# Performance work log

Hardware: AMD Instinct MI355X
Metric: run time of the kernel (lower is better)

The kernel has to match this reference:

```python
import jax, jax.numpy as jnp
import numpy as np

H, DH, D, S, B = 8, 64, 512, 512, 2
EPS = 1e-5

def _trop_linear(x, W):
    # y[..., o] = max_i (x[..., i] + W[o, i])
    return jnp.max(x[..., None, :] + W, axis=-1)

def _layer_norm(x, gamma, beta):
    mu = jnp.mean(x, axis=-1, keepdims=True)
    var = jnp.mean((x - mu) ** 2, axis=-1, keepdims=True)
    return (x - mu) * jax.lax.rsqrt(var + EPS) * gamma + beta

def setup_inputs() -> dict:
    key = jax.random.key(0)
    ks = jax.random.split(key, 8)
    sc = lambda fan_in: 1.0 / np.sqrt(fan_in)
    return {
        "h":   jax.random.normal(ks[0], (S, B, D), jnp.float32),
        "Wq":  jax.random.normal(ks[1], (H * DH, D), jnp.float32) * sc(D),
        "Wkv": jax.random.normal(ks[2], (2 * H * DH, D), jnp.float32) * sc(D),
        "Wqt": jax.random.normal(ks[3], (DH, DH), jnp.float32),
        "Wkt": jax.random.normal(ks[4], (DH, DH), jnp.float32),
        "Wvt": jax.random.normal(ks[5], (DH, DH), jnp.float32),
        "lam": jnp.ones((1, 1, D), jnp.float32),
        "Wo":  jax.random.normal(ks[6], (D, H * DH), jnp.float32) * sc(H * DH),
        "gamma": jnp.ones((D,), jnp.float32),
        "beta":  jnp.zeros((D,), jnp.float32),
    }

def reference(h, Wq, Wkv, Wqt, Wkt, Wvt, lam, Wo, gamma, beta):
    # h: [S, B, D]; mems=None so c == h; pre_lnorm=False
    c = h
    head_q = h @ Wq.T                                # [S, B, H*DH]
    kv = c @ Wkv.T                                   # [S, B, 2*H*DH]
    head_k, head_v = jnp.split(kv, 2, axis=-1)

    norm = lambda x: jnp.log1p(jax.nn.relu(x)) - lam  # tropical normalize
    head_q, head_k, head_v = norm(head_q), norm(head_k), norm(head_v)

    # [S,B,H,DH] -> [B,S,H,DH] -> flat reshape to [B*H, S, DH] (matches torch)
    to_bh = lambda x: jnp.transpose(x.reshape(S, B, H, DH), (1, 0, 2, 3)).reshape(B * H, S, DH)
    q = _trop_linear(to_bh(head_q), Wqt)
    k = _trop_linear(to_bh(head_k), Wkt)
    v = _trop_linear(to_bh(head_v), Wvt)

    # tropical distance score: -(max_d(q-k) - min_d(q-k)) over head dim
    diff = q[:, :, None, :] - k[:, None, :, :]        # [BH, Sq, Sk, DH]
    attn_scores = -(jnp.max(diff, axis=-1) - jnp.min(diff, axis=-1))  # [BH,Sq,Sk]

    # max-plus aggregation: context = max_sk(score + v)
    sum_sv = attn_scores[..., None] + v[:, None, :, :]  # [BH, Sq, Sk, DH]
    context = jnp.max(sum_sv, axis=2)                   # [BH, Sq, DH]

    # flat reshape back (matches torch), permute, expm1
    context = context.reshape(B, H, S, DH)
    context = jnp.transpose(context, (2, 0, 1, 3))      # [S, B, H, DH]
    context = jnp.expm1(context)
    attn_vec = context.reshape(S, B, H * DH)

    attn_out = attn_vec @ Wo.T                          # [S, B, D]
    return _layer_norm(h + attn_out, gamma, beta)
```

## Files before the change

### kernel.cpp

```cpp
#include <hip/hip_runtime.h>
#include <cmath>

typedef __attribute__((ext_vector_type(8))) __bf16 bf16x8;
typedef __attribute__((ext_vector_type(4))) float f32x4;

namespace {
constexpr int GP = 512;
constexpr int WS_Q = 0;
constexpr int WS_K = 524288;
constexpr int WS_V = 1048576;
}

__device__ inline unsigned short f2bf(float x) {
  union { float f; unsigned u; } v; v.f = x;
  unsigned r = v.u + 0x7fff + ((v.u >> 16) & 1);
  return (unsigned short)(r >> 16);
}

__device__ inline void cvt8_store(unsigned short* dst, float4 a, float4 b) {
  ushort4 lo, hi;
  lo.x = f2bf(a.x); lo.y = f2bf(a.y); lo.z = f2bf(a.z); lo.w = f2bf(a.w);
  hi.x = f2bf(b.x); hi.y = f2bf(b.y); hi.z = f2bf(b.z); hi.w = f2bf(b.w);
  *(ushort4*)dst = lo; *(ushort4*)(dst + 4) = hi;
}

__global__ __launch_bounds__(256) void k_gemm0t(const float* __restrict__ h,
    const float* __restrict__ Wq, const float* __restrict__ Wkv,
    const float* __restrict__ lam, const float* __restrict__ Wqt,
    const float* __restrict__ Wkt, const float* __restrict__ Wvt,
    float* __restrict__ qkv)
{
  __shared__ unsigned short As[64][72];
  __shared__ unsigned short Bs[64][72];
  __shared__ float Wl[64][65];
  __shared__ float nl[64][68];
  const int tid = threadIdx.x;
  const int bx = blockIdx.x;
  const int r0 = blockIdx.y * 64, c0 = bx * 64;
  const int which = c0 >> 9;
  const int hh = bx & 7;
  const float* Wt = (which == 0) ? Wqt : (which == 1) ? Wkt : Wvt;
  #pragma unroll
  for (int q = 0; q < 16; ++q) {
    int idx = q * 256 + tid;
    Wl[idx >> 6][idx & 63] = Wt[idx];
  }
  const int w = tid >> 6, l = tid & 63;
  const int wr = (w >> 1) * 32, wc = (w & 1) * 32;
  const int srow = tid >> 3, sk8 = (tid & 7) * 8;
  f32x4 acc[2][2] = {};
  for (int kk = 0; kk < 512; kk += 64) {
    __syncthreads();
    #pragma unroll
    for (int q2 = 0; q2 < 2; ++q2) {
      int row = srow + q2 * 32;
      const float* ap = &h[(r0 + row) * 512 + kk + sk8];
      cvt8_store(&As[row][sk8], *(const float4*)ap, *(const float4*)(ap + 4));
      int c = c0 + row;
      const float* wrp = (c < 512) ? (Wq + c * 512) : (Wkv + (c - 512) * 512);
      cvt8_store(&Bs[row][sk8], *(const float4*)&wrp[kk + sk8],
                 *(const float4*)&wrp[kk + sk8 + 4]);
    }
    __syncthreads();
    #pragma unroll
    for (int ks = 0; ks < 2; ++ks) {
      const int kc = ks * 32 + (l >> 4) * 8;
      bf16x8 a0 = *(const bf16x8*)&As[wr +      (l & 15)][kc];
      bf16x8 a1 = *(const bf16x8*)&As[wr + 16 + (l & 15)][kc];
      bf16x8 b0 = *(const bf16x8*)&Bs[wc +      (l & 15)][kc];
      bf16x8 b1 = *(const bf16x8*)&Bs[wc + 16 + (l & 15)][kc];
      acc[0][0] = __builtin_amdgcn_mfma_f32_16x16x32_bf16(a0, b0, acc[0][0], 0, 0, 0);
      acc[0][1] = __builtin_amdgcn_mfma_f32_16x16x32_bf16(a0, b1, acc[0][1], 0, 0, 0);
      acc[1][0] = __builtin_amdgcn_mfma_f32_16x16x32_bf16(a1, b0, acc[1][0], 0, 0, 0);
      acc[1][1] = __builtin_amdgcn_mfma_f32_16x16x32_bf16(a1, b1, acc[1][1], 0, 0, 0);
    }
  }
  #pragma unroll
  for (int i = 0; i < 2; ++i)
    #pragma unroll
    for (int j = 0; j < 2; ++j)
      #pragma unroll
      for (int r = 0; r < 4; ++r) {
        int rl = wr + i * 16 + (l >> 4) * 4 + r;
        int cl = wc + j * 16 + (l & 15);
        nl[rl][cl] = log1pf(fmaxf(acc[i][j][r], 0.f)) - lam[hh * 64 + cl];
      }
  __syncthreads();
  float wreg[64];
  #pragma unroll
  for (int i = 0; i < 64; ++i) wreg[i] = Wl[l][i];
  #pragma unroll 2
  for (int it = 0; it < 16; ++it) {
    int lr = w + it * 4;
    float m0 = -INFINITY, m1 = -INFINITY, m2 = -INFINITY, m3 = -INFINITY;
    #pragma unroll
    for (int i = 0; i < 64; i += 4) {
      f32x4 nv = *(const f32x4*)&nl[lr][i];
      m0 = fmaxf(m0, nv[0] + wreg[i]);
      m1 = fmaxf(m1, nv[1] + wreg[i + 1]);
      m2 = fmaxf(m2, nv[2] + wreg[i + 2]);
      m3 = fmaxf(m3, nv[3] + wreg[i + 3]);
    }
    int r = r0 + lr;
    int s = r >> 1, bb = r & 1;
    int g = bb * 8 + (s >> 6);
    int p = ((s & 63) << 3) | hh;
    qkv[which * 524288 + ((g << 9) + p) * 64 + l] =
        fmaxf(fmaxf(m0, m1), fmaxf(m2, m3));
  }
}

__global__ __launch_bounds__(256) void k_attn(const float* __restrict__ qkv,
    float* __restrict__ ctxp)
{
  const int pt = blockIdx.x;
  const int g  = blockIdx.y;
  const int cs = blockIdx.z;
  const float* qb = qkv + WS_Q + g * GP * 64;
  const float* kb = qkv + WS_K + g * GP * 64;
  const float* vb = qkv + WS_V + g * GP * 64;
  __shared__ float qs[32][64];
  __shared__ float ks[64][64];
  __shared__ float vs[64][64];
  __shared__ float ss[32][68];
  const int tid = threadIdx.x;
  const int tr = tid >> 4, tc = tid & 15;
  const int xb = tc & 7;
  #pragma unroll
  for (int q2 = 0; q2 < 2; ++q2) {
    int row = tr + q2 * 16;
    f32x4 v4 = *(const f32x4*)&qb[(pt * 32 + row) * 64 + tc * 4];
    *(f32x4*)&qs[row][((tc ^ (row & 7))) * 4] = v4;
  }
  float ctx[2][4];
  #pragma unroll
  for (int i = 0; i < 2; ++i)
    #pragma unroll
    for (int j = 0; j < 4; ++j) ctx[i][j] = -INFINITY;

  for (int cc = 0; cc < 2; ++cc) {
    const int c0 = cs * 128 + cc * 64;
    __syncthreads();
    #pragma unroll
    for (int q4 = 0; q4 < 4; ++q4) {
      int row = tr + q4 * 16;
      int sb = (tc ^ (row & 7)) * 4;
      *(f32x4*)&ks[row][sb] = *(const f32x4*)&kb[(c0 + row) * 64 + tc * 4];
      *(f32x4*)&vs[row][sb] = *(const f32x4*)&vb[(c0 + row) * 64 + tc * 4];
    }
    __syncthreads();
    float mx[2][4], mn[2][4];
    #pragma unroll
    for (int i = 0; i < 2; ++i)
      #pragma unroll
      for (int m = 0; m < 4; ++m) { mx[i][m] = -INFINITY; mn[i][m] = INFINITY; }
    const int r0 = tr * 2, r1 = r0 + 1;
    #pragma unroll 2
    for (int b = 0; b < 16; ++b) {
      f32x4 q0 = *(const f32x4*)&qs[r0][(b ^ (r0 & 7)) * 4];
      f32x4 q1 = *(const f32x4*)&qs[r1][(b ^ (r1 & 7)) * 4];
      const int kblk = (b ^ xb) * 4;
      #pragma unroll
      for (int m = 0; m < 4; ++m) {
        f32x4 kv = *(const f32x4*)&ks[tc + m * 16][kblk];
        #pragma unroll
        for (int e = 0; e < 4; ++e) {
          float d0 = q0[e] - kv[e];
          float d1 = q1[e] - kv[e];
          mx[0][m] = fmaxf(mx[0][m], d0); mn[0][m] = fminf(mn[0][m], d0);
          mx[1][m] = fmaxf(mx[1][m], d1); mn[1][m] = fminf(mn[1][m], d1);
        }
      }
    }
    #pragma unroll
    for (int i = 0; i < 2; ++i)
      #pragma unroll
      for (int m = 0; m < 4; ++m)
        ss[tr * 2 + i][tc + m * 16] = mn[i][m] - mx[i][m];
    __syncthreads();
    #pragma unroll 2
    for (int cb = 0; cb < 16; ++cb) {
      f32x4 s0 = *(const f32x4*)&ss[r0][cb * 4];
      f32x4 s1 = *(const f32x4*)&ss[r1][cb * 4];
      #pragma unroll
      for (int e = 0; e < 4; ++e) {
        int c = cb * 4 + e;
        f32x4 vv = *(const f32x4*)&vs[c][(tc ^ (c & 7)) * 4];
        #pragma unroll
        for (int j = 0; j < 4; ++j) {
          ctx[0][j] = fmaxf(ctx[0][j], s0[e] + vv[j]);
          ctx[1][j] = fmaxf(ctx[1][j], s1[e] + vv[j]);
        }
      }
    }
  }
  int base = cs * 524288 + g * 32768 + (pt * 32 + tr * 2) * 64 + tc * 4;
  f32x4 o0, o1;
  #pragma unroll
  for (int j = 0; j < 4; ++j) { o0[j] = ctx[0][j]; o1[j] = ctx[1][j]; }
  *(f32x4*)&ctxp[base]      = o0;
  *(f32x4*)&ctxp[base + 64] = o1;
}

__global__ __launch_bounds__(256) void k_gemm1c(const float* __restrict__ ctxp,
    const float* __restrict__ Wo, float* __restrict__ ao)
{
  __shared__ unsigned short As[64][72];
  __shared__ unsigned short Bs[64][72];
  const int tid = threadIdx.x;
  const int r0 = blockIdx.y * 64, c0 = blockIdx.x * 64;
  const int w = tid >> 6, l = tid & 63;
  const int wr = (w >> 1) * 32, wc = (w & 1) * 32;
  const int srow = tid >> 3, sk8 = (tid & 7) * 8;
  f32x4 acc[2][2] = {};
  for (int kk = 0; kk < 512; kk += 64) {
    __syncthreads();
    #pragma unroll
    for (int q2 = 0; q2 < 2; ++q2) {
      int row = srow + q2 * 32;
      int r = r0 + row;
      int p = r >> 1, b2 = r & 1;
      int j0 = kk + sk8;
      int h2 = j0 >> 6, d0 = j0 & 63;
      const float* cp = ctxp + (b2 * 8 + h2) * 32768 + p * 64 + d0;
      f32x4 m0 = *(const f32x4*)cp;
      f32x4 m1 = *(const f32x4*)(cp + 4);
      #pragma unroll
      for (int cs = 1; cs < 4; ++cs) {
        f32x4 a0 = *(const f32x4*)(cp + cs * 524288);
        f32x4 a1 = *(const f32x4*)(cp + cs * 524288 + 4);
        #pragma unroll
        for (int e = 0; e < 4; ++e) {
          m0[e] = fmaxf(m0[e], a0[e]);
          m1[e] = fmaxf(m1[e], a1[e]);
        }
      }
      ushort4 lo, hi;
      lo.x = f2bf(expm1f(m0[0])); lo.y = f2bf(expm1f(m0[1]));
      lo.z = f2bf(expm1f(m0[2])); lo.w = f2bf(expm1f(m0[3]));
      hi.x = f2bf(expm1f(m1[0])); hi.y = f2bf(expm1f(m1[1]));
      hi.z = f2bf(expm1f(m1[2])); hi.w = f2bf(expm1f(m1[3]));
      *(ushort4*)&As[row][sk8] = lo;
      *(ushort4*)&As[row][sk8 + 4] = hi;
      const float* bp = &Wo[(c0 + row) * 512 + kk + sk8];
      cvt8_store(&Bs[row][sk8], *(const float4*)bp, *(const float4*)(bp + 4));
    }
    __syncthreads();
    #pragma unroll
    for (int ks = 0; ks < 2; ++ks) {
      const int kc = ks * 32 + (l >> 4) * 8;
      bf16x8 a0 = *(const bf16x8*)&As[wr +      (l & 15)][kc];
      bf16x8 a1 = *(const bf16x8*)&As[wr + 16 + (l & 15)][kc];
      bf16x8 b0 = *(const bf16x8*)&Bs[wc +      (l & 15)][kc];
      bf16x8 b1 = *(const bf16x8*)&Bs[wc + 16 + (l & 15)][kc];
      acc[0][0] = __builtin_amdgcn_mfma_f32_16x16x32_bf16(a0, b0, acc[0][0], 0, 0, 0);
      acc[0][1] = __builtin_amdgcn_mfma_f32_16x16x32_bf16(a0, b1, acc[0][1], 0, 0, 0);
      acc[1][0] = __builtin_amdgcn_mfma_f32_16x16x32_bf16(a1, b0, acc[1][0], 0, 0, 0);
      acc[1][1] = __builtin_amdgcn_mfma_f32_16x16x32_bf16(a1, b1, acc[1][1], 0, 0, 0);
    }
  }
  #pragma unroll
  for (int i = 0; i < 2; ++i)
    #pragma unroll
    for (int j = 0; j < 2; ++j)
      #pragma unroll
      for (int r = 0; r < 4; ++r) {
        int row = r0 + wr + i * 16 + (l >> 4) * 4 + r;
        int col = c0 + wc + j * 16 + (l & 15);
        ao[row * 512 + col] = acc[i][j][r];
      }
}

__global__ __launch_bounds__(256) void k_ln(const float* __restrict__ hin,
    const float* __restrict__ ao, const float* __restrict__ gamma,
    const float* __restrict__ beta, float* __restrict__ outp)
{
  const int r = blockIdx.x;
  const int tid = threadIdx.x;
  float2 hv = *(const float2*)&hin[r * 512 + tid * 2];
  float2 a2 = *(const float2*)&ao[r * 512 + tid * 2];
  float x0 = hv.x + a2.x, x1 = hv.y + a2.y;
  float sum = x0 + x1;
  float sq = x0 * x0 + x1 * x1;
  #pragma unroll
  for (int o = 32; o > 0; o >>= 1) {
    sum += __shfl_down(sum, o);
    sq  += __shfl_down(sq, o);
  }
  __shared__ float rs[8];
  const int lane = tid & 63, w = tid >> 6;
  if (lane == 0) { rs[w] = sum; rs[4 + w] = sq; }
  __syncthreads();
  float tot   = rs[0] + rs[1] + rs[2] + rs[3];
  float totsq = rs[4] + rs[5] + rs[6] + rs[7];
  float mu  = tot * (1.f / 512.f);
  float var = totsq * (1.f / 512.f) - mu * mu;
  float rstd = rsqrtf(fmaxf(var, 0.f) + 1e-5f);
  int c0 = tid * 2;
  outp[r * 512 + c0]     = (x0 - mu) * rstd * gamma[c0]     + beta[c0];
  outp[r * 512 + c0 + 1] = (x1 - mu) * rstd * gamma[c0 + 1] + beta[c0 + 1];
}

extern "C" void kernel_launch(void* const* d_in, const int* in_sizes, int n_in,
                              void* d_out, int out_size, void* d_ws, size_t ws_size,
                              hipStream_t stream) {
  const float* hin   = (const float*)d_in[0];
  const float* Wq    = (const float*)d_in[1];
  const float* Wkv   = (const float*)d_in[2];
  const float* Wqt   = (const float*)d_in[3];
  const float* Wkt   = (const float*)d_in[4];
  const float* Wvt   = (const float*)d_in[5];
  const float* lam   = (const float*)d_in[6];
  const float* Wo    = (const float*)d_in[7];
  const float* gamma = (const float*)d_in[8];
  const float* beta  = (const float*)d_in[9];
  char* wsb = (char*)d_ws;
  float* qkvbuf = (float*)wsb;
  float* ctxp   = (float*)(wsb + 6291456);
  float* ao     = (float*)wsb;
  float* out    = (float*)d_out;

  k_gemm0t<<<dim3(24, 16),    256, 0, stream>>>(hin, Wq, Wkv, lam, Wqt, Wkt, Wvt, qkvbuf);
  k_attn  <<<dim3(16, 16, 4), 256, 0, stream>>>(qkvbuf, ctxp);
  k_gemm1c<<<dim3(8, 16),     256, 0, stream>>>(ctxp, Wo, ao);
  k_ln    <<<dim3(1024),      256, 0, stream>>>(hin, ao, gamma, beta, out);
}
```

Baseline: 83.86 us.

## Enlarge attention query tile to 4x4 register block and use one wave per LayerNorm row

The attention kernel now processes 64 query rows per block instead of 32, giving each thread a 4x4 register tile of queries by keys. K and V values loaded from LDS are reused across four query rows, and the grid is halved. The LayerNorm kernel assigns one wavefront per row with vectorized loads and an xor-shuffle reduction, which removes the shared-memory barrier. The tropical-linear inner loop is also reshaped into fewer max chains. The cost is higher register use in attention, which may reduce occupancy, and fewer blocks to spread across the GPU.

```diff
diff --git a/kernel.cpp b/kernel.cpp
--- a/kernel.cpp
+++ b/kernel.cpp
@@ -92,21 +92,20 @@
   #pragma unroll 2
   for (int it = 0; it < 16; ++it) {
     int lr = w + it * 4;
-    float m0 = -INFINITY, m1 = -INFINITY, m2 = -INFINITY, m3 = -INFINITY;
+    float m0 = -INFINITY, m1 = -INFINITY;
     #pragma unroll
     for (int i = 0; i < 64; i += 4) {
       f32x4 nv = *(const f32x4*)&nl[lr][i];
-      m0 = fmaxf(m0, nv[0] + wreg[i]);
-      m1 = fmaxf(m1, nv[1] + wreg[i + 1]);
-      m2 = fmaxf(m2, nv[2] + wreg[i + 2]);
-      m3 = fmaxf(m3, nv[3] + wreg[i + 3]);
+      float t0 = nv[0] + wreg[i],     t1 = nv[1] + wreg[i + 1];
+      float t2 = nv[2] + wreg[i + 2], t3 = nv[3] + wreg[i + 3];
+      m0 = fmaxf(fmaxf(m0, t0), t1);
+      m1 = fmaxf(fmaxf(m1, t2), t3);
     }
     int r = r0 + lr;
     int s = r >> 1, bb = r & 1;
     int g = bb * 8 + (s >> 6);
     int p = ((s & 63) << 3) | hh;
-    qkv[which * 524288 + ((g << 9) + p) * 64 + l] =
-        fmaxf(fmaxf(m0, m1), fmaxf(m2, m3));
+    qkv[which * 524288 + ((g << 9) + p) * 64 + l] = fmaxf(m0, m1);
   }
 }
 
@@ -119,25 +118,25 @@
   const float* qb = qkv + WS_Q + g * GP * 64;
   const float* kb = qkv + WS_K + g * GP * 64;
   const float* vb = qkv + WS_V + g * GP * 64;
-  __shared__ float qs[32][64];
+  __shared__ float qs[64][64];
   __shared__ float ks[64][64];
   __shared__ float vs[64][64];
-  __shared__ float ss[32][68];
+  __shared__ float ss[64][68];
   const int tid = threadIdx.x;
   const int tr = tid >> 4, tc = tid & 15;
-  const int xb = tc & 7;
-  #pragma unroll
-  for (int q2 = 0; q2 < 2; ++q2) {
-    int row = tr + q2 * 16;
-    f32x4 v4 = *(const f32x4*)&qb[(pt * 32 + row) * 64 + tc * 4];
-    *(f32x4*)&qs[row][((tc ^ (row & 7))) * 4] = v4;
-  }
-  float ctx[2][4];
-  #pragma unroll
-  for (int i = 0; i < 2; ++i)
+  #pragma unroll
+  for (int q4 = 0; q4 < 4; ++q4) {
+    int row = tr + q4 * 16;
+    *(f32x4*)&qs[row][(tc ^ (row & 7)) * 4] =
+        *(const f32x4*)&qb[(pt * 64 + row) * 64 + tc * 4];
+  }
+  float ctx[4][4];
+  #pragma unroll
+  for (int i = 0; i < 4; ++i)
     #pragma unroll
     for (int j = 0; j < 4; ++j) ctx[i][j] = -INFINITY;
 
+  const int xq0 = (4 * tr) & 7;
   for (int cc = 0; cc < 2; ++cc) {
     const int c0 = cs * 128 + cc * 64;
     __syncthreads();
@@ -149,57 +148,73 @@
       *(f32x4*)&vs[row][sb] = *(const f32x4*)&vb[(c0 + row) * 64 + tc * 4];
     }
     __syncthreads();
-    float mx[2][4], mn[2][4];
-    #pragma unroll
-    for (int i = 0; i < 2; ++i)
+    float mx[4][4], mn[4][4];
+    #pragma unroll
+    for (int i = 0; i < 4; ++i)
       #pragma unroll
       for (int m = 0; m < 4; ++m) { mx[i][m] = -INFINITY; mn[i][m] = INFINITY; }
-    const int r0 = tr * 2, r1 = r0 + 1;
-    #pragma unroll 2
+    #pragma unroll 4
     for (int b = 0; b < 16; ++b) {
-      f32x4 q0 = *(const f32x4*)&qs[r0][(b ^ (r0 & 7)) * 4];
-      f32x4 q1 = *(const f32x4*)&qs[r1][(b ^ (r1 & 7)) * 4];
-      const int kblk = (b ^ xb) * 4;
-      #pragma unroll
-      for (int m = 0; m < 4; ++m) {
-        f32x4 kv = *(const f32x4*)&ks[tc + m * 16][kblk];
+      f32x4 qv[4], kv[4];
+      #pragma unroll
+      for (int i = 0; i < 4; ++i)
+        qv[i] = *(const f32x4*)&qs[4 * tr + i][(b ^ ((xq0 + i) & 7)) * 4];
+      const int kblk = (b ^ (tc & 7)) * 4;
+      #pragma unroll
+      for (int m = 0; m < 4; ++m)
+        kv[m] = *(const f32x4*)&ks[tc + 16 * m][kblk];
+      #pragma unroll
+      for (int i = 0; i < 4; ++i)
         #pragma unroll
-        for (int e = 0; e < 4; ++e) {
-          float d0 = q0[e] - kv[e];
-          float d1 = q1[e] - kv[e];
-          mx[0][m] = fmaxf(mx[0][m], d0); mn[0][m] = fminf(mn[0][m], d0);
-          mx[1][m] = fmaxf(mx[1][m], d1); mn[1][m] = fminf(mn[1][m], d1);
+        for (int m = 0; m < 4; ++m) {
+          float d0 = qv[i][0] - kv[m][0];
+          float d1 = qv[i][1] - kv[m][1];
+          float d2 = qv[i][2] - kv[m][2];
+          float d3 = qv[i][3] - kv[m][3];
+          mx[i][m] = fmaxf(fmaxf(mx[i][m], d0), d1);
+          mn[i][m] = fminf(fminf(mn[i][m], d0), d1);
+          mx[i][m] = fmaxf(fmaxf(mx[i][m], d2), d3);
+          mn[i][m] = fminf(fminf(mn[i][m], d2), d3);
         }
-      }
-    }
-    #pragma unroll
-    for (int i = 0; i < 2; ++i)
+    }
+    #pragma unroll
+    for (int i = 0; i < 4; ++i)
       #pragma unroll
       for (int m = 0; m < 4; ++m)
-        ss[tr * 2 + i][tc + m * 16] = mn[i][m] - mx[i][m];
-    __syncthreads();
-    #pragma unroll 2
+        ss[4 * tr + i][tc + 16 * m] = mn[i][m] - mx[i][m];
+    __syncthreads();
+    #pragma unroll 4
     for (int cb = 0; cb < 16; ++cb) {
-      f32x4 s0 = *(const f32x4*)&ss[r0][cb * 4];
-      f32x4 s1 = *(const f32x4*)&ss[r1][cb * 4];
+      f32x4 sv[4], vv[4];
+      #pragma unroll
+      for (int i = 0; i < 4; ++i)
+        sv[i] = *(const f32x4*)&ss[4 * tr + i][cb * 4];
       #pragma unroll
       for (int e = 0; e < 4; ++e) {
         int c = cb * 4 + e;
-        f32x4 vv = *(const f32x4*)&vs[c][(tc ^ (c & 7)) * 4];
+        vv[e] = *(const f32x4*)&vs[c][(tc ^ (c & 7)) * 4];
+      }
+      #pragma unroll
+      for (int i = 0; i < 4; ++i) {
         #pragma unroll
-        for (int j = 0; j < 4; ++j) {
-          ctx[0][j] = fmaxf(ctx[0][j], s0[e] + vv[j]);
-          ctx[1][j] = fmaxf(ctx[1][j], s1[e] + vv[j]);
-        }
-      }
-    }
-  }
-  int base = cs * 524288 + g * 32768 + (pt * 32 + tr * 2) * 64 + tc * 4;
-  f32x4 o0, o1;
-  #pragma unroll
-  for (int j = 0; j < 4; ++j) { o0[j] = ctx[0][j]; o1[j] = ctx[1][j]; }
-  *(f32x4*)&ctxp[base]      = o0;
-  *(f32x4*)&ctxp[base + 64] = o1;
+        for (int j = 0; j < 4; ++j)
+          ctx[i][j] = fmaxf(fmaxf(ctx[i][j], sv[i][0] + vv[0][j]),
+                            sv[i][1] + vv[1][j]);
+        #pragma unroll
+        for (int j = 0; j < 4; ++j)
+          ctx[i][j] = fmaxf(fmaxf(ctx[i][j], sv[i][2] + vv[2][j]),
+                            sv[i][3] + vv[3][j]);
+      }
+    }
+  }
+  int base = cs * 524288 + g * 32768 + (pt * 64 + 4 * tr) * 64 + tc * 4;
+  #pragma unroll
+  for (int i = 0; i < 4; ++i) {
+    f32x4 o;
+    #pragma unroll
+    for (int j = 0; j < 4; ++j) o[j] = ctx[i][j];
+    *(f32x4*)&ctxp[base + i * 64] = o;
+  }
 }
 
 __global__ __launch_bounds__(256) void k_gemm1c(const float* __restrict__ ctxp,
@@ -275,30 +290,35 @@
     const float* __restrict__ ao, const float* __restrict__ gamma,
     const float* __restrict__ beta, float* __restrict__ outp)
 {
-  const int r = blockIdx.x;
-  const int tid = threadIdx.x;
-  float2 hv = *(const float2*)&hin[r * 512 + tid * 2];
-  float2 a2 = *(const float2*)&ao[r * 512 + tid * 2];
-  float x0 = hv.x + a2.x, x1 = hv.y + a2.y;
-  float sum = x0 + x1;
-  float sq = x0 * x0 + x1 * x1;
+  const int r = blockIdx.x * 4 + (threadIdx.x >> 6);
+  const int lane = threadIdx.x & 63;
+  const int c0 = lane * 8;
+  f32x4 h0 = *(const f32x4*)&hin[r * 512 + c0];
+  f32x4 h1 = *(const f32x4*)&hin[r * 512 + c0 + 4];
+  f32x4 a0 = *(const f32x4*)&ao[r * 512 + c0];
+  f32x4 a1 = *(const f32x4*)&ao[r * 512 + c0 + 4];
+  float x[8];
+  #pragma unroll
+  for (int e = 0; e < 4; ++e) { x[e] = h0[e] + a0[e]; x[4 + e] = h1[e] + a1[e]; }
+  float sum = 0.f, sq = 0.f;
+  #pragma unroll
+  for (int e = 0; e < 8; ++e) { sum += x[e]; sq += x[e] * x[e]; }
   #pragma unroll
   for (int o = 32; o > 0; o >>= 1) {
-    sum += __shfl_down(sum, o);
-    sq  += __shfl_down(sq, o);
-  }
-  __shared__ float rs[8];
-  const int lane = tid & 63, w = tid >> 6;
-  if (lane == 0) { rs[w] = sum; rs[4 + w] = sq; }
-  __syncthreads();
-  float tot   = rs[0] + rs[1] + rs[2] + rs[3];
-  float totsq = rs[4] + rs[5] + rs[6] + rs[7];
-  float mu  = tot * (1.f / 512.f);
-  float var = totsq * (1.f / 512.f) - mu * mu;
+    sum += __shfl_xor(sum, o);
+    sq  += __shfl_xor(sq, o);
+  }
+  float mu  = sum * (1.f / 512.f);
+  float var = sq * (1.f / 512.f) - mu * mu;
   float rstd = rsqrtf(fmaxf(var, 0.f) + 1e-5f);
-  int c0 = tid * 2;
-  outp[r * 512 + c0]     = (x0 - mu) * rstd * gamma[c0]     + beta[c0];
-  outp[r * 512 + c0 + 1] = (x1 - mu) * rstd * gamma[c0 + 1] + beta[c0 + 1];
+  f32x4 o0, o1;
+  #pragma unroll
+  for (int e = 0; e < 4; ++e) {
+    o0[e] = (x[e]     - mu) * rstd * gamma[c0 + e]     + beta[c0 + e];
+    o1[e] = (x[4 + e] - mu) * rstd * gamma[c0 + 4 + e] + beta[c0 + 4 + e];
+  }
+  *(f32x4*)&outp[r * 512 + c0]     = o0;
+  *(f32x4*)&outp[r * 512 + c0 + 4] = o1;
 }
 
 extern "C" void kernel_launch(void* const* d_in, const int* in_sizes, int n_in,
@@ -320,8 +340,8 @@
   float* ao     = (float*)wsb;
   float* out    = (float*)d_out;
 
-  k_gemm0t<<<dim3(24, 16),    256, 0, stream>>>(hin, Wq, Wkv, lam, Wqt, Wkt, Wvt, qkvbuf);
-  k_attn  <<<dim3(16, 16, 4), 256, 0, stream>>>(qkvbuf, ctxp);
-  k_gemm1c<<<dim3(8, 16),     256, 0, stream>>>(ctxp, Wo, ao);
-  k_ln    <<<dim3(1024),      256, 0, stream>>>(hin, ao, gamma, beta, out);
-}
+  k_gemm0t<<<dim3(24, 16),   256, 0, stream>>>(hin, Wq, Wkv, lam, Wqt, Wkt, Wvt, qkvbuf);
+  k_attn  <<<dim3(8, 16, 4), 256, 0, stream>>>(qkvbuf, ctxp);
+  k_gemm1c<<<dim3(8, 16),    256, 0, stream>>>(ctxp, Wo, ao);
+  k_ln    <<<dim3(256),      256, 0, stream>>>(hin, ao, gamma, beta, out);
+}
```

Result: faster. 80.76 us (-3.7%).
